# Kernel tuning notes

Measured on AMD Instinct MI355X. Metric: run time of the kernel, lower is better.

## Reference

```python
import jax, jax.numpy as jnp
import numpy as np

KH, KW = 3, 3          # kernel_size
SH, SW = 1, 1          # strides
EM_ITERS = 3           # standard EM routing iteration count
EPS = 1e-9


def to_blocks(x):
    """im2col-style block extraction matching ConvCaps2D._to_blocks.
    x: [B, H, W, ...] -> [B, Ho, Wo, KH, KW, ...] with Ho=(H-KH+1)//SH."""
    Ho = (x.shape[1] - KH + 1) // SH
    Wo = (x.shape[2] - KW + 1) // SW
    rows = []
    for i in range(KH):
        cols = [x[:, i:i + (Ho - 1) * SH + 1:SH, j:j + (Wo - 1) * SW + 1:SW]
                for j in range(KW)]
        rows.append(jnp.stack(cols, axis=3))   # [B,Ho,Wo,KW,...]
    return jnp.stack(rows, axis=3)             # [B,Ho,Wo,KH,KW,...]


def em_routing(votes, a_in, beta_a, beta_u):
    """EM routing (Hinton et al. 2018 matrix capsules).
    votes: [B,Ho,Wo,O,N,D], a_in: [B,Ho,Wo,N], beta_*: [1,1,1,O].
    Returns poses mu [B,Ho,Wo,O,D], activations [B,Ho,Wo,O]."""
    B, Ho, Wo, O, N, D = votes.shape
    R = jnp.full((B, Ho, Wo, O, N), 1.0 / O, dtype=votes.dtype)
    a = a_in[:, :, :, None, :]                                  # [B,Ho,Wo,1,N]
    mu = None
    a_out = None
    for t in range(EM_ITERS):
        inv_temp = 1.0 + t                                      # increasing lambda schedule
        # ---- M-step ----
        r = R * a                                               # [B,Ho,Wo,O,N]
        r_sum = jnp.sum(r, axis=-1, keepdims=True) + EPS        # [B,Ho,Wo,O,1]
        mu = jnp.einsum('bhwon,bhwond->bhwod', r, votes) / r_sum
        diff2 = (votes - mu[:, :, :, :, None, :]) ** 2          # [B,Ho,Wo,O,N,D]
        sigma2 = jnp.einsum('bhwon,bhwond->bhwod', r, diff2) / r_sum + EPS
        cost = jnp.sum((beta_u[..., None] + 0.5 * jnp.log(sigma2)) * r_sum, axis=-1)
        a_out = jax.nn.sigmoid(inv_temp * (beta_a - cost))      # [B,Ho,Wo,O]
        # ---- E-step (skipped after last M-step) ----
        if t < EM_ITERS - 1:
            s2 = sigma2[:, :, :, :, None, :]
            logp = -0.5 * jnp.sum(jnp.log(2.0 * jnp.pi * s2) + diff2 / s2, axis=-1)
            logits = jnp.log(a_out + EPS)[..., None] + logp     # [B,Ho,Wo,O,N]
            R = jax.nn.softmax(logits, axis=3)                  # normalize over output caps
    return mu, a_out


def setup_inputs() -> dict:
    key = jax.random.key(0)
    k1, k2, k3, k4, k5 = jax.random.split(key, 5)
    B, H, W, Cin, d1, d2 = 4, 16, 16, 16, 4, 4
    O = 32
    poses = jax.random.normal(k1, (B, H, W, Cin, d1, d2), dtype=jnp.float32)
    activations = jax.random.uniform(k2, (B, H, W, Cin), dtype=jnp.float32)
    fan_in = KH * KW * Cin * d1 * d2
    kernel = jax.random.normal(k3, (O, KH, KW, Cin, d1, d2), dtype=jnp.float32) * np.sqrt(2.0 / fan_in).astype(np.float32)
    beta_a = jax.random.normal(k4, (1, 1, 1, O), dtype=jnp.float32) * 0.1
    beta_u = jax.random.normal(k5, (1, 1, 1, O), dtype=jnp.float32) * 0.1
    return {"poses": poses, "activations": activations, "kernel": kernel,
            "beta_a": beta_a, "beta_u": beta_u}


def reference(poses, activations, kernel, beta_a, beta_u):
    B, _, _, Cin, d1, d2 = poses.shape
    O = kernel.shape[0]
    pose_blocks = to_blocks(poses)                              # [B,Ho,Wo,KH,KW,Cin,d1,d2]
    # votes = pose @ W per (output channel, kernel offset, input channel)
    votes = jnp.einsum('bhwKLcij,oKLcjl->bhwoKLcil', pose_blocks, kernel)
    Ho, Wo = votes.shape[1], votes.shape[2]
    N = KH * KW * Cin
    votes = votes.reshape(B, Ho, Wo, O, N, d1 * d2)             # [B,Ho,Wo,O,N,D]
    a_blocks = to_blocks(activations).reshape(B, Ho, Wo, N)
    mu, a_out = em_routing(votes, a_blocks, beta_a, beta_u)
    capsule_poses = mu.reshape(B, Ho, Wo, O, d1, d2)
    return capsule_poses, a_out
```

## Files before the change

### kernel.cpp

```cpp
#include <hip/hip_runtime.h>
#include <math.h>

#define NBLK 784
#define O_ 32
#define N_ 144
#define D_ 16
#define PS 20
#define RS 148

__global__ __launch_bounds__(256) void convcaps_em(
    const float* __restrict__ poses,
    const float* __restrict__ acts,
    const float* __restrict__ kern,
    const float* __restrict__ beta_a,
    const float* __restrict__ beta_u,
    float* __restrict__ out)
{
    const int pix = blockIdx.x;
    const int b  = pix / 196;
    const int hw = pix - b * 196;
    const int ho = hw / 14;
    const int wo = hw - ho * 14;

    __shared__ __align__(16) float P[N_ * PS];
    __shared__ float A[N_];
    __shared__ float Rm[O_ * RS];

    const int t = threadIdx.x;

    for (int idx = t; idx < N_ * D_; idx += 256) {
        int n = idx >> 4, d = idx & 15;
        int ki = n / 48, kj = (n >> 4) - ki * 3, c = n & 15;
        P[n * PS + d] = poses[((b * 16 + ho + ki) * 16 + (wo + kj)) * 256 + c * 16 + d];
    }
    if (t < N_) {
        int n = t;
        int ki = n / 48, kj = (n >> 4) - ki * 3, c = n & 15;
        A[n] = acts[((b * 16 + ho + ki) * 16 + (wo + kj)) * 16 + c];
    }
    for (int idx = t; idx < O_ * N_; idx += 256) {
        int oo = idx / N_;
        int nn = idx - oo * N_;
        Rm[oo * RS + nn] = 0.03125f;
    }
    __syncthreads();

    const int o = t >> 3;
    const int s = t & 7;
    const float bu = beta_u[o];
    const float ba = beta_a[o];
    const float* Kbase = kern + (size_t)o * (N_ * D_);

    float a_out = 0.f;
    float mu[16];

    for (int it = 0; it < 3; ++it) {
        float S1[16], S2[16];
#pragma unroll
        for (int d = 0; d < 16; ++d) { S1[d] = 0.f; S2[d] = 0.f; }
        float rs = 0.f;

        for (int k = 0; k < 18; ++k) {
            const int n = s + (k << 3);
            const float r = Rm[o * RS + n] * A[n];
            rs += r;
            float pv[16], kv[16];
            const float4* Pp = (const float4*)(P + n * PS);
            ((float4*)pv)[0] = Pp[0];
            ((float4*)pv)[1] = Pp[1];
            ((float4*)pv)[2] = Pp[2];
            ((float4*)pv)[3] = Pp[3];
            const float4* Kp = (const float4*)(Kbase + n * D_);
            ((float4*)kv)[0] = Kp[0];
            ((float4*)kv)[1] = Kp[1];
            ((float4*)kv)[2] = Kp[2];
            ((float4*)kv)[3] = Kp[3];
#pragma unroll
            for (int i = 0; i < 4; ++i) {
#pragma unroll
                for (int l = 0; l < 4; ++l) {
                    float v = fmaf(pv[i*4+0], kv[0+l],
                              fmaf(pv[i*4+1], kv[4+l],
                              fmaf(pv[i*4+2], kv[8+l],
                                   pv[i*4+3] * kv[12+l])));
                    S1[i*4+l] = fmaf(r, v, S1[i*4+l]);
                    S2[i*4+l] = fmaf(r * v, v, S2[i*4+l]);
                }
            }
        }

#pragma unroll
        for (int m = 1; m < 8; m <<= 1) {
            rs += __shfl_xor(rs, m, 64);
#pragma unroll
            for (int d = 0; d < 16; ++d) {
                S1[d] += __shfl_xor(S1[d], m, 64);
                S2[d] += __shfl_xor(S2[d], m, 64);
            }
        }

        rs += 1e-9f;
        const float inv_rs = 1.0f / rs;
        float sig[16];
#pragma unroll
        for (int d = 0; d < 16; ++d) {
            mu[d] = S1[d] * inv_rs;
            sig[d] = fmaf(-mu[d], mu[d], S2[d] * inv_rs) + 1e-9f;
        }
        float lpart = logf(sig[2*s]) + logf(sig[2*s+1]);
#pragma unroll
        for (int m = 1; m < 8; m <<= 1) lpart += __shfl_xor(lpart, m, 64);
        const float L = lpart;
        const float cost = rs * fmaf(0.5f, L, 16.0f * bu);
        const float x = (float)(it + 1) * (ba - cost);
        a_out = 1.0f / (1.0f + expf(-x));

        if (it < 2) {
            float isig[16];
#pragma unroll
            for (int d = 0; d < 16; ++d) isig[d] = 1.0f / sig[d];
            const float LC = logf(a_out + 1e-9f)
                           - 0.5f * (16.0f * 1.8378770664093453f + L);
            __syncthreads();

            for (int k = 0; k < 18; ++k) {
                const int n = s + (k << 3);
                float pv[16], kv[16];
                const float4* Pp = (const float4*)(P + n * PS);
                ((float4*)pv)[0] = Pp[0];
                ((float4*)pv)[1] = Pp[1];
                ((float4*)pv)[2] = Pp[2];
                ((float4*)pv)[3] = Pp[3];
                const float4* Kp = (const float4*)(Kbase + n * D_);
                ((float4*)kv)[0] = Kp[0];
                ((float4*)kv)[1] = Kp[1];
                ((float4*)kv)[2] = Kp[2];
                ((float4*)kv)[3] = Kp[3];
                float Q = 0.f;
#pragma unroll
                for (int i = 0; i < 4; ++i) {
#pragma unroll
                    for (int l = 0; l < 4; ++l) {
                        float v = fmaf(pv[i*4+0], kv[0+l],
                                  fmaf(pv[i*4+1], kv[4+l],
                                  fmaf(pv[i*4+2], kv[8+l],
                                       pv[i*4+3] * kv[12+l])));
                        const float df = v - mu[i*4+l];
                        Q = fmaf(df * df, isig[i*4+l], Q);
                    }
                }
                Rm[o * RS + n] = fmaf(-0.5f, Q, LC);
            }
            __syncthreads();

            if (t < N_) {
                float v[32];
                float mx = -1e30f;
#pragma unroll
                for (int oo = 0; oo < 32; ++oo) {
                    v[oo] = Rm[oo * RS + t];
                    mx = fmaxf(mx, v[oo]);
                }
                float sm = 0.f;
#pragma unroll
                for (int oo = 0; oo < 32; ++oo) {
                    v[oo] = expf(v[oo] - mx);
                    sm += v[oo];
                }
                const float inv = 1.0f / sm;
#pragma unroll
                for (int oo = 0; oo < 32; ++oo)
                    Rm[oo * RS + t] = v[oo] * inv;
            }
            __syncthreads();
        }
    }

    float2 w2;
    w2.x = mu[2 * s];
    w2.y = mu[2 * s + 1];
    *(float2*)(out + (size_t)pix * 512 + o * 16 + 2 * s) = w2;
    if (s == 0) out[401408 + pix * 32 + o] = a_out;
}

extern "C" void kernel_launch(void* const* d_in, const int* in_sizes, int n_in,
                              void* d_out, int out_size, void* d_ws, size_t ws_size,
                              hipStream_t stream)
{
    const float* poses  = (const float*)d_in[0];
    const float* acts   = (const float*)d_in[1];
    const float* kern   = (const float*)d_in[2];
    const float* beta_a = (const float*)d_in[3];
    const float* beta_u = (const float*)d_in[4];
    float* out = (float*)d_out;
    convcaps_em<<<NBLK, 256, 0, stream>>>(poses, acts, kern, beta_a, beta_u, out);
}
```

Baseline: 110.7 us.

## Double-buffer vote loads, use fast math intrinsics, raise occupancy hint

```diff
diff --git a/kernel.cpp b/kernel.cpp
--- a/kernel.cpp
+++ b/kernel.cpp
@@ -8,7 +8,62 @@
 #define PS 20
 #define RS 148
 
-__global__ __launch_bounds__(256) void convcaps_em(
+#define LD(kk, rr, pvv, kvv) do {                                          \
+    const int n_ = s + ((kk) << 3);                                        \
+    rr = Rm[o * RS + n_] * A[n_];                                          \
+    const float4* Pp_ = (const float4*)(P + n_ * PS);                      \
+    ((float4*)(pvv))[0] = Pp_[0]; ((float4*)(pvv))[1] = Pp_[1];            \
+    ((float4*)(pvv))[2] = Pp_[2]; ((float4*)(pvv))[3] = Pp_[3];            \
+    const float4* Kp_ = (const float4*)(Kbase + n_ * D_);                  \
+    ((float4*)(kvv))[0] = Kp_[0]; ((float4*)(kvv))[1] = Kp_[1];            \
+    ((float4*)(kvv))[2] = Kp_[2]; ((float4*)(kvv))[3] = Kp_[3];            \
+} while (0)
+
+#define LD2(kk, pvv, kvv) do {                                             \
+    const int n_ = s + ((kk) << 3);                                        \
+    const float4* Pp_ = (const float4*)(P + n_ * PS);                      \
+    ((float4*)(pvv))[0] = Pp_[0]; ((float4*)(pvv))[1] = Pp_[1];            \
+    ((float4*)(pvv))[2] = Pp_[2]; ((float4*)(pvv))[3] = Pp_[3];            \
+    const float4* Kp_ = (const float4*)(Kbase + n_ * D_);                  \
+    ((float4*)(kvv))[0] = Kp_[0]; ((float4*)(kvv))[1] = Kp_[1];            \
+    ((float4*)(kvv))[2] = Kp_[2]; ((float4*)(kvv))[3] = Kp_[3];            \
+} while (0)
+
+#define ACC(rr, pvv, kvv) do {                                             \
+    rs += rr;                                                              \
+    _Pragma("unroll")                                                      \
+    for (int i_ = 0; i_ < 4; ++i_) {                                       \
+      _Pragma("unroll")                                                    \
+      for (int l_ = 0; l_ < 4; ++l_) {                                     \
+        float v_ = fmaf((pvv)[i_*4+0], (kvv)[0+l_],                        \
+                   fmaf((pvv)[i_*4+1], (kvv)[4+l_],                        \
+                   fmaf((pvv)[i_*4+2], (kvv)[8+l_],                        \
+                        (pvv)[i_*4+3] * (kvv)[12+l_])));                   \
+        S1[i_*4+l_] = fmaf(rr, v_, S1[i_*4+l_]);                           \
+        S2[i_*4+l_] = fmaf(rr * v_, v_, S2[i_*4+l_]);                      \
+      }                                                                    \
+    }                                                                      \
+} while (0)
+
+#define QWR(kk, pvv, kvv) do {                                             \
+    const int n_ = s + ((kk) << 3);                                        \
+    float Q_ = 0.f;                                                        \
+    _Pragma("unroll")                                                      \
+    for (int i_ = 0; i_ < 4; ++i_) {                                       \
+      _Pragma("unroll")                                                    \
+      for (int l_ = 0; l_ < 4; ++l_) {                                     \
+        float v_ = fmaf((pvv)[i_*4+0], (kvv)[0+l_],                        \
+                   fmaf((pvv)[i_*4+1], (kvv)[4+l_],                        \
+                   fmaf((pvv)[i_*4+2], (kvv)[8+l_],                        \
+                        (pvv)[i_*4+3] * (kvv)[12+l_])));                   \
+        const float df_ = v_ - mu[i_*4+l_];                                \
+        Q_ = fmaf(df_ * df_, isg[i_*4+l_], Q_);                            \
+      }                                                                    \
+    }                                                                      \
+    Rm[o * RS + n_] = fmaf(-0.5f, Q_, LC);                                 \
+} while (0)
+
+__global__ __launch_bounds__(256, 3) void convcaps_em(
     const float* __restrict__ poses,
     const float* __restrict__ acts,
     const float* __restrict__ kern,
@@ -47,7 +102,7 @@
 
     const int o = t >> 3;
     const int s = t & 7;
-    const float bu = beta_u[o];
+    const float buv = beta_u[o];
     const float ba = beta_a[o];
     const float* Kbase = kern + (size_t)o * (N_ * D_);
 
@@ -60,32 +115,15 @@
         for (int d = 0; d < 16; ++d) { S1[d] = 0.f; S2[d] = 0.f; }
         float rs = 0.f;
 
-        for (int k = 0; k < 18; ++k) {
-            const int n = s + (k << 3);
-            const float r = Rm[o * RS + n] * A[n];
-            rs += r;
-            float pv[16], kv[16];
-            const float4* Pp = (const float4*)(P + n * PS);
-            ((float4*)pv)[0] = Pp[0];
-            ((float4*)pv)[1] = Pp[1];
-            ((float4*)pv)[2] = Pp[2];
-            ((float4*)pv)[3] = Pp[3];
-            const float4* Kp = (const float4*)(Kbase + n * D_);
-            ((float4*)kv)[0] = Kp[0];
-            ((float4*)kv)[1] = Kp[1];
-            ((float4*)kv)[2] = Kp[2];
-            ((float4*)kv)[3] = Kp[3];
-#pragma unroll
-            for (int i = 0; i < 4; ++i) {
-#pragma unroll
-                for (int l = 0; l < 4; ++l) {
-                    float v = fmaf(pv[i*4+0], kv[0+l],
-                              fmaf(pv[i*4+1], kv[4+l],
-                              fmaf(pv[i*4+2], kv[8+l],
-                                   pv[i*4+3] * kv[12+l])));
-                    S1[i*4+l] = fmaf(r, v, S1[i*4+l]);
-                    S2[i*4+l] = fmaf(r * v, v, S2[i*4+l]);
-                }
+        {
+            float rA, rB;
+            float pvA[16], kvA[16], pvB[16], kvB[16];
+            LD(0, rA, pvA, kvA);
+            for (int k2 = 0; k2 < 9; ++k2) {
+                LD(2 * k2 + 1, rB, pvB, kvB);
+                ACC(rA, pvA, kvA);
+                if (k2 < 8) LD(2 * k2 + 2, rA, pvA, kvA);
+                ACC(rB, pvB, kvB);
             }
         }
 
@@ -107,49 +145,30 @@
             mu[d] = S1[d] * inv_rs;
             sig[d] = fmaf(-mu[d], mu[d], S2[d] * inv_rs) + 1e-9f;
         }
-        float lpart = logf(sig[2*s]) + logf(sig[2*s+1]);
+        float lpart = __logf(sig[2 * s] * sig[2 * s + 1]);
 #pragma unroll
         for (int m = 1; m < 8; m <<= 1) lpart += __shfl_xor(lpart, m, 64);
         const float L = lpart;
-        const float cost = rs * fmaf(0.5f, L, 16.0f * bu);
+        const float cost = rs * fmaf(0.5f, L, 16.0f * buv);
         const float x = (float)(it + 1) * (ba - cost);
-        a_out = 1.0f / (1.0f + expf(-x));
+        a_out = 1.0f / (1.0f + __expf(-x));
 
         if (it < 2) {
-            float isig[16];
-#pragma unroll
-            for (int d = 0; d < 16; ++d) isig[d] = 1.0f / sig[d];
-            const float LC = logf(a_out + 1e-9f)
+            float isg[16];
+#pragma unroll
+            for (int d = 0; d < 16; ++d) isg[d] = 1.0f / sig[d];
+            const float LC = __logf(a_out + 1e-9f)
                            - 0.5f * (16.0f * 1.8378770664093453f + L);
+
+            float pvA[16], kvA[16], pvB[16], kvB[16];
+            LD2(0, pvA, kvA);
             __syncthreads();
 
-            for (int k = 0; k < 18; ++k) {
-                const int n = s + (k << 3);
-                float pv[16], kv[16];
-                const float4* Pp = (const float4*)(P + n * PS);
-                ((float4*)pv)[0] = Pp[0];
-                ((float4*)pv)[1] = Pp[1];
-                ((float4*)pv)[2] = Pp[2];
-                ((float4*)pv)[3] = Pp[3];
-                const float4* Kp = (const float4*)(Kbase + n * D_);
-                ((float4*)kv)[0] = Kp[0];
-                ((float4*)kv)[1] = Kp[1];
-                ((float4*)kv)[2] = Kp[2];
-                ((float4*)kv)[3] = Kp[3];
-                float Q = 0.f;
-#pragma unroll
-                for (int i = 0; i < 4; ++i) {
-#pragma unroll
-                    for (int l = 0; l < 4; ++l) {
-                        float v = fmaf(pv[i*4+0], kv[0+l],
-                                  fmaf(pv[i*4+1], kv[4+l],
-                                  fmaf(pv[i*4+2], kv[8+l],
-                                       pv[i*4+3] * kv[12+l])));
-                        const float df = v - mu[i*4+l];
-                        Q = fmaf(df * df, isig[i*4+l], Q);
-                    }
-                }
-                Rm[o * RS + n] = fmaf(-0.5f, Q, LC);
+            for (int k2 = 0; k2 < 9; ++k2) {
+                LD2(2 * k2 + 1, pvB, kvB);
+                QWR(2 * k2, pvA, kvA);
+                if (k2 < 8) LD2(2 * k2 + 2, pvA, kvA);
+                QWR(2 * k2 + 1, pvB, kvB);
             }
             __syncthreads();
 
@@ -164,7 +183,7 @@
                 float sm = 0.f;
 #pragma unroll
                 for (int oo = 0; oo < 32; ++oo) {
-                    v[oo] = expf(v[oo] - mx);
+                    v[oo] = __expf(v[oo] - mx);
                     sm += v[oo];
                 }
                 const float inv = 1.0f / sm;
```

Measured after the change: 116.6 us. +5.4%, slower.
